# Optimization experiments

Hardware: AMD Instinct MI355X
Metric: run time of the kernel (lower is better)

## Reference

```python
import jax, jax.numpy as jnp
import numpy as np

N_HEAD, D_HEAD, D_MODEL, D_INNER, KSIZE = 16, 64, 1024, 4096, 3
LN_EPS = 1e-3  # keras LayerNormalization default epsilon


def _layernorm(x, g, b):
    m = jnp.mean(x, axis=-1, keepdims=True)
    v = jnp.var(x, axis=-1, keepdims=True)
    return (x - m) * jax.lax.rsqrt(v + LN_EPS) * g + b


def _conv1d_same(x, w, b):
    # x: [B, S, Cin], w: [K, Cin, Cout] (keras Conv1D layout)
    y = jax.lax.conv_general_dilated(x, w, window_strides=(1,), padding='SAME',
                                     dimension_numbers=('NWC', 'WIO', 'NWC'))
    return y + b


def setup_inputs() -> dict:
    key = jax.random.key(0)
    ks = jax.random.split(key, 12)
    B, S, D = 4, 1024, D_MODEL
    dec_inp = jax.random.normal(ks[0], (B, S, D), dtype=jnp.float32)
    # padding mask: True = valid token; ensure >=1 padded position per row
    lengths = jax.random.randint(ks[1], (B,), S // 2, S)
    mask = (jnp.arange(S)[None, :] < lengths[:, None])[:, :, None]  # [B,S,1] bool
    sd = 0.02
    qkv_w = jax.random.normal(ks[2], (D, 3 * N_HEAD * D_HEAD), dtype=jnp.float32) * sd
    qkv_b = jnp.zeros((3 * N_HEAD * D_HEAD,), dtype=jnp.float32)
    o_w = jax.random.normal(ks[3], (N_HEAD * D_HEAD, D), dtype=jnp.float32) * sd
    ln1_g = jnp.ones((D,), dtype=jnp.float32)
    ln1_b = jnp.zeros((D,), dtype=jnp.float32)
    conv1_w = jax.random.normal(ks[4], (KSIZE, D, D_INNER), dtype=jnp.float32) * sd
    conv1_b = jnp.zeros((D_INNER,), dtype=jnp.float32)
    conv2_w = jax.random.normal(ks[5], (KSIZE, D_INNER, D), dtype=jnp.float32) * sd
    conv2_b = jnp.zeros((D,), dtype=jnp.float32)
    ln2_g = jnp.ones((D,), dtype=jnp.float32)
    ln2_b = jnp.zeros((D,), dtype=jnp.float32)
    return dict(dec_inp=dec_inp, mask=mask, qkv_w=qkv_w, qkv_b=qkv_b, o_w=o_w,
                ln1_g=ln1_g, ln1_b=ln1_b, conv1_w=conv1_w, conv1_b=conv1_b,
                conv2_w=conv2_w, conv2_b=conv2_b, ln2_g=ln2_g, ln2_b=ln2_b)


def _forward(dec_inp, mask, qkv_w, qkv_b, o_w, ln1_g, ln1_b,
             conv1_w, conv1_b, conv2_w, conv2_b, ln2_g, ln2_b):
    B, S, D = dec_inp.shape
    H, dh = N_HEAD, D_HEAD
    scale = 1.0 / (dh ** 0.5)
    # --- MultiHeadAttn (post-lnorm; dropout inactive at inference) ---
    residual = dec_inp
    qkv = dec_inp @ qkv_w + qkv_b                       # [B,S,3*H*dh]
    hq, hk, hv = jnp.split(qkv, 3, axis=2)
    to_flat = lambda h: h.reshape(B, S, H, dh).transpose(0, 2, 1, 3).reshape(B * H, S, dh)
    q, k, v = to_flat(hq), to_flat(hk), to_flat(hv)
    score = jnp.einsum('bqd,bkd->bqk', q, k) * scale    # [B*H, S, S]
    # attn_mask = ~mask.squeeze(2): True at PAD positions (faithful to TF port)
    am = (~mask[:, :, 0]).astype(score.dtype)[:, None, :]    # [B,1,S]
    am = jnp.tile(am, (H, S, 1))                             # [B*H,S,S] (tile over batch axis, as in tf.tile)
    add = jnp.where(am.astype(bool), am, -jnp.inf)           # pad -> +1.0, valid -> -inf (as written in source)
    score = score + add
    prob = jax.nn.softmax(score, axis=2)
    vec = prob @ v                                      # [B*H,S,dh]
    # faithful to source reshapes: [B*H,S,dh] -> [H,B,S,dh] -> [B,S,H*dh]
    vec = vec.reshape(H, B, S, dh).transpose(1, 2, 0, 3).reshape(B, S, H * dh)
    attn_out = vec @ o_w
    out = _layernorm(residual + attn_out, ln1_g, ln1_b)
    # mask-multiply between blocks
    out = out * mask.astype(out.dtype)
    # --- PositionwiseConvFF (post-lnorm) ---
    core = _conv1d_same(out, conv1_w, conv1_b)
    core = jax.nn.relu(core)
    core = _conv1d_same(core, conv2_w, conv2_b)
    out = _layernorm(out + core, ln2_g, ln2_b)
    out = out * mask.astype(out.dtype)
    return out


def reference(dec_inp, mask, qkv_w, qkv_b, o_w, ln1_g, ln1_b,
              conv1_w, conv1_b, conv2_w, conv2_b, ln2_g, ln2_b):
    return _forward(dec_inp, mask, qkv_w, qkv_b, o_w, ln1_g, ln1_b,
                    conv1_w, conv1_b, conv2_w, conv2_b, ln2_g, ln2_b)
```

## Files before the change

### kernel.cpp

```cpp
#include <hip/hip_runtime.h>
#include <cstdint>
#include <cstddef>

typedef float f32x4 __attribute__((ext_vector_type(4)));
typedef __bf16 bf16x8 __attribute__((ext_vector_type(8)));
typedef unsigned short u16;

__device__ __forceinline__ float bf2f(u16 u) {
  union { unsigned int i; float f; } x; x.i = ((unsigned int)u) << 16; return x.f;
}
__device__ __forceinline__ u16 f2bf(float f) {
  union { float f; unsigned int i; } x; x.f = f;
  unsigned int i = x.i;
  i += 0x7fffu + ((i >> 16) & 1u);
  return (u16)(i >> 16);
}

#if defined(__has_builtin)
#if __has_builtin(__builtin_amdgcn_global_load_lds)
#define HAS_GLL 1
#endif
#endif

__device__ __forceinline__ void async16(const u16* g, u16* l) {
#ifdef HAS_GLL
  __builtin_amdgcn_global_load_lds((const __attribute__((address_space(1))) void*)(const void*)g,
                                   (__attribute__((address_space(3))) void*)(void*)l, 16, 0, 0);
#else
  *(uint4*)l = *(const uint4*)g;
#endif
}

__global__ void compact_mask(const unsigned char* __restrict__ mask,
                             int* __restrict__ padIdx, int* __restrict__ padCnt,
                             float* __restrict__ maskf) {
  const int b = blockIdx.x;
  const int lane = threadIdx.x;
  int stride = 1;
  if (mask[1] == 0) stride = (mask[4] != 0) ? 4 : 8;
  int cnt = 0;
  for (int s0 = 0; s0 < 1024; s0 += 64) {
    const int s = s0 + lane;
    const bool valid = (mask[(size_t)((b << 10) + s) * stride] != 0);
    maskf[(b << 10) + s] = valid ? 1.f : 0.f;
    const bool pad = !valid;
    const unsigned long long bal = __ballot(pad);
    const int rank = (int)__popcll(bal & ((1ull << lane) - 1ull));
    if (pad) padIdx[(b << 10) + cnt + rank] = s;
    cnt += (int)__popcll(bal);
  }
  if (lane == 0) padCnt[b] = cnt;
}

__global__ __launch_bounds__(256)
void f32_to_bf16(const float* __restrict__ in, u16* __restrict__ out, int n4) {
  const int i = blockIdx.x * 256 + threadIdx.x;
  if (i < n4) {
    const float4 v = ((const float4*)in)[i];
    u16 o[4] = { f2bf(v.x), f2bf(v.y), f2bf(v.z), f2bf(v.w) };
    ((ushort4*)out)[i] = *(const ushort4*)o;
  }
}

__global__ __launch_bounds__(256)
void transpose_f32_bf16(const float* __restrict__ in, u16* __restrict__ out, int R, int C) {
  __shared__ u16 tile[64][65];
  const int r0 = blockIdx.y << 6, c0 = blockIdx.x << 6;
  const int tid = threadIdx.x;
  const int lr = tid >> 3, lc = (tid & 7) << 3;
#pragma unroll
  for (int p = 0; p < 2; ++p) {
    const int row = lr + (p << 5);
    const float4 a = *(const float4*)(in + (size_t)(r0 + row) * C + c0 + lc);
    const float4 bq = *(const float4*)(in + (size_t)(r0 + row) * C + c0 + lc + 4);
    tile[row][lc + 0] = f2bf(a.x); tile[row][lc + 1] = f2bf(a.y);
    tile[row][lc + 2] = f2bf(a.z); tile[row][lc + 3] = f2bf(a.w);
    tile[row][lc + 4] = f2bf(bq.x); tile[row][lc + 5] = f2bf(bq.y);
    tile[row][lc + 6] = f2bf(bq.z); tile[row][lc + 7] = f2bf(bq.w);
  }
  __syncthreads();
#pragma unroll
  for (int p = 0; p < 2; ++p) {
    const int oc = lr + (p << 5);
    u16 tmp[8];
#pragma unroll
    for (int e = 0; e < 8; ++e) tmp[e] = tile[lc + e][oc];
    *(uint4*)(out + (size_t)(c0 + oc) * R + r0 + lc) = *(const uint4*)tmp;
  }
}

template<int NTAPS, bool RELU, int SPLITK>
__global__ __launch_bounds__(256)
void gemm_bt(const u16* __restrict__ A, const u16* __restrict__ BT,
             const float* __restrict__ bias, u16* __restrict__ C, u16* __restrict__ Calt,
             int M, int N, int Korig, const u16* __restrict__ zp) {
  __shared__ __align__(16) u16 As[128 * 64];
  __shared__ __align__(16) u16 Bs[128 * 64];
  const int tid = threadIdx.x;
  const int m0 = blockIdx.y << 7;
  const int n0 = blockIdx.x << 7;
  const int kz = (SPLITK > 1) ? blockIdx.z : 0;
  const int Ktot = NTAPS * Korig;
  const int kchunk = Ktot / SPLITK;
  const int lane = tid & 63;
  const int w = tid >> 6;
  const int wm = (w >> 1) << 6;
  const int wn = (w & 1) << 6;
  const int fr = lane & 15;
  const int quad = lane >> 4;
  const int srow = tid >> 3;
  const int scol = (tid & 7) << 3;
  const int sx = (((tid & 7) ^ (srow & 7)) << 3);

  f32x4 acc[4][4] = {};

  const int kbeg = kz * kchunk, kend = kbeg + kchunk;
  for (int k0 = kbeg; k0 < kend; k0 += 64) {
    int t = 0, c0 = k0;
    if (NTAPS == 3) { t = k0 / Korig; c0 = k0 - t * Korig; }
#pragma unroll
    for (int i = 0; i < 4; ++i) {
      const int row = srow + (i << 5);
      const u16* src;
      if (NTAPS == 3) {
        const int m = m0 + row;
        const int sp = (m & 1023) + t - 1;
        src = ((unsigned)sp < 1024u) ? (A + (size_t)(m + t - 1) * Korig + c0 + sx)
                                     : (zp + ((tid & 255) << 3));
      } else {
        src = A + (size_t)(m0 + row) * Korig + c0 + sx;
      }
      async16(src, &As[(row << 6) + scol]);
    }
#pragma unroll
    for (int i = 0; i < 4; ++i) {
      const int n = srow + (i << 5);
      async16(BT + (size_t)(n0 + n) * Ktot + k0 + sx, &Bs[(n << 6) + scol]);
    }
    asm volatile("s_waitcnt vmcnt(0)" ::: "memory");
    __syncthreads();
#pragma unroll
    for (int ks = 0; ks < 64; ks += 32) {
      const int ccol = ((((ks >> 3) + quad) ^ (fr & 7)) << 3);
      bf16x8 af[4], bfr[4];
#pragma unroll
      for (int mi = 0; mi < 4; ++mi)
        af[mi] = *(const bf16x8*)&As[((wm + (mi << 4) + fr) << 6) + ccol];
#pragma unroll
      for (int ni = 0; ni < 4; ++ni)
        bfr[ni] = *(const bf16x8*)&Bs[((wn + (ni << 4) + fr) << 6) + ccol];
#pragma unroll
      for (int mi = 0; mi < 4; ++mi)
#pragma unroll
        for (int ni = 0; ni < 4; ++ni)
          acc[mi][ni] = __builtin_amdgcn_mfma_f32_16x16x32_bf16(af[mi], bfr[ni], acc[mi][ni], 0, 0, 0);
    }
    __syncthreads();
  }
  const int rbase = m0 + wm + (quad << 2);
  const int cbase = n0 + wn + fr;
  u16* dst = C;
  if (SPLITK > 1 && kz > 0) dst = Calt + (size_t)(kz - 1) * ((size_t)M * N);
#pragma unroll
  for (int ni = 0; ni < 4; ++ni) {
    const int col = cbase + (ni << 4);
    const float bv = (SPLITK == 1 && bias) ? bias[col] : 0.f;
#pragma unroll
    for (int mi = 0; mi < 4; ++mi) {
#pragma unroll
      for (int r = 0; r < 4; ++r) {
        float v = acc[mi][ni][r] + bv;
        if (RELU) v = fmaxf(v, 0.f);
        dst[(size_t)(rbase + (mi << 4) + r) * N + col] = f2bf(v);
      }
    }
  }
}

__global__ __launch_bounds__(256)
void reduce_split4(const u16* __restrict__ P0, const u16* __restrict__ P1,
                   const float* __restrict__ bias, u16* __restrict__ out,
                   int MN, int Ncols) {
  const int i8 = (blockIdx.x * 256 + threadIdx.x) << 3;
  if (i8 >= MN) return;
  const uint4 a = *(const uint4*)(P0 + i8);
  const uint4 b = *(const uint4*)(P1 + i8);
  const uint4 c = *(const uint4*)(P1 + MN + i8);
  const uint4 d = *(const uint4*)(P1 + 2 * MN + i8);
  const u16 *ua = (const u16*)&a, *ub = (const u16*)&b, *uc = (const u16*)&c, *ud = (const u16*)&d;
  const int cb = i8 & (Ncols - 1);
  u16 o[8];
#pragma unroll
  for (int e = 0; e < 8; ++e) {
    const float s = bf2f(ua[e]) + bf2f(ub[e]) + bf2f(uc[e]) + bf2f(ud[e]) + bias[cb + e];
    o[e] = f2bf(s);
  }
  *(uint4*)(out + i8) = *(const uint4*)o;
}

__global__ __launch_bounds__(256)
void gather_v(const u16* __restrict__ qkv, const int* __restrict__ padIdx,
              const int* __restrict__ padCnt, u16* __restrict__ Vt) {
  const int bm = blockIdx.x;
  const int jt = blockIdx.y;
  const int b = bm >> 2, mb = bm & 3;
  const int npad = padCnt[mb];
  const int npadR = (npad + 63) & ~63;
  if (jt * 64 >= npadR) return;
  const int tid = threadIdx.x;
  __shared__ int rows[64];
  if (tid < 64) {
    const int j = jt * 64 + tid;
    const int jj = j < npad ? j : npad - 1;
    rows[tid] = padIdx[(mb << 10) + jj];
  }
  __shared__ u16 tile[64][72];
  for (int c = 0; c < 16; ++c) {
    const int ch0 = c << 6;
    __syncthreads();
#pragma unroll
    for (int p = 0; p < 2; ++p) {
      const int r = (tid >> 3) + (p << 5);
      const int ch = (tid & 7) << 3;
      const uint4 v = *(const uint4*)(qkv + (size_t)((b << 10) + rows[r]) * 3072 + 2048 + ch0 + ch);
      const u16* us = (const u16*)&v;
#pragma unroll
      for (int e = 0; e < 8; ++e) tile[r][ch + e] = us[e];
    }
    __syncthreads();
#pragma unroll
    for (int p = 0; p < 2; ++p) {
      const int r = (tid >> 3) + (p << 5);
      const int jc = (tid & 7) << 3;
      u16 tmp[8];
#pragma unroll
      for (int e = 0; e < 8; ++e) tmp[e] = tile[jc + e][r];
      *(uint4*)(Vt + (size_t)((bm << 10) + ch0 + r) * 512 + jt * 64 + jc) = *(const uint4*)tmp;
    }
  }
}

__global__ __launch_bounds__(256)
void attn_mfma(const u16* __restrict__ qkv, const u16* __restrict__ Vt,
               const int* __restrict__ padIdx, const int* __restrict__ padCnt,
               u16* __restrict__ vecS) {
  __shared__ __align__(16) u16 Ks[64 * 64];
  __shared__ __align__(16) u16 Vts[64 * 64];
  __shared__ __align__(16) u16 Ps[4][32 * 88];
  __shared__ int rowsIdx[512];
  const int i = blockIdx.x;
  const int qt = blockIdx.y;
  const int b = i >> 4, h = i & 15;
  const int mb = h & 3, bm = (b << 2) + mb;
  const int h_out = i >> 2;
  const int npad = padCnt[mb];
  const int nkt = (npad + 63) >> 6;
  const int tid = threadIdx.x;
  const int w = tid >> 6, lane = tid & 63;
  const int fr = lane & 15, quad = lane >> 4, fko = quad << 3;
  const int srow = tid >> 3, scol = (tid & 7) << 3;
  const int sx = (((tid & 7) ^ (srow & 7)) << 3);

#pragma unroll
  for (int p = 0; p < 2; ++p) {
    const int j = (p << 8) + tid;
    const int jj = j < npad ? j : npad - 1;
    rowsIdx[j] = padIdx[(mb << 10) + jj];
  }

  const int qw = (qt << 7) + (w << 5);
  bf16x8 qf[2][2];
#pragma unroll
  for (int rt = 0; rt < 2; ++rt)
#pragma unroll
    for (int ks = 0; ks < 2; ++ks)
      qf[rt][ks] = *(const bf16x8*)(qkv + (size_t)((b << 10) + qw + (rt << 4) + fr) * 3072 +
                                    (h << 6) + (ks << 5) + fko);

  f32x4 O[2][4];
  float mrun[2][4], lrun[2][4];
#pragma unroll
  for (int rt = 0; rt < 2; ++rt)
#pragma unroll
    for (int r = 0; r < 4; ++r) {
      mrun[rt][r] = -1e30f; lrun[rt][r] = 0.f;
#pragma unroll
      for (int dt = 0; dt < 4; ++dt) O[rt][dt][r] = 0.f;
    }
  __syncthreads();

  for (int kt = 0; kt < nkt; ++kt) {
#pragma unroll
    for (int p = 0; p < 2; ++p) {
      const int r = srow + (p << 5);
      const int grow = rowsIdx[(kt << 6) + r];
      async16(qkv + (size_t)((b << 10) + grow) * 3072 + 1024 + (h << 6) + sx,
              &Ks[(r << 6) + scol]);
      async16(Vt + (size_t)((bm << 10) + (h << 6) + r) * 512 + (kt << 6) + sx,
              &Vts[(r << 6) + scol]);
    }
    asm volatile("s_waitcnt vmcnt(0)" ::: "memory");
    __syncthreads();

    f32x4 S[2][4];
#pragma unroll
    for (int rt = 0; rt < 2; ++rt)
#pragma unroll
      for (int nt = 0; nt < 4; ++nt)
#pragma unroll
        for (int r = 0; r < 4; ++r) S[rt][nt][r] = 0.f;
#pragma unroll
    for (int ks = 0; ks < 2; ++ks) {
      const int ccol = ((((ks << 2) + quad) ^ (fr & 7)) << 3);
      bf16x8 bfr[4];
#pragma unroll
      for (int nt = 0; nt < 4; ++nt)
        bfr[nt] = *(const bf16x8*)&Ks[(((nt << 4) + fr) << 6) + ccol];
#pragma unroll
      for (int rt = 0; rt < 2; ++rt)
#pragma unroll
        for (int nt = 0; nt < 4; ++nt)
          S[rt][nt] = __builtin_amdgcn_mfma_f32_16x16x32_bf16(qf[rt][ks], bfr[nt], S[rt][nt], 0, 0, 0);
    }

#pragma unroll
    for (int nt = 0; nt < 4; ++nt) {
      const int key = (kt << 6) + (nt << 4) + fr;
      const bool dead = (key >= npad);
#pragma unroll
      for (int rt = 0; rt < 2; ++rt)
#pragma unroll
        for (int r = 0; r < 4; ++r) {
          float s = S[rt][nt][r] * 0.125f;
          S[rt][nt][r] = dead ? -1e30f : s;
        }
    }

#pragma unroll
    for (int rt = 0; rt < 2; ++rt) {
#pragma unroll
      for (int r = 0; r < 4; ++r) {
        float mx = fmaxf(fmaxf(S[rt][0][r], S[rt][1][r]), fmaxf(S[rt][2][r], S[rt][3][r]));
#pragma unroll
        for (int off = 1; off <= 8; off <<= 1) mx = fmaxf(mx, __shfl_xor(mx, off, 64));
        const float mnew = fmaxf(mrun[rt][r], mx);
        const float alpha = __expf(mrun[rt][r] - mnew);
        mrun[rt][r] = mnew;
        float rsum = 0.f;
#pragma unroll
        for (int nt = 0; nt < 4; ++nt) {
          const float p_ = __expf(S[rt][nt][r] - mnew);
          S[rt][nt][r] = p_;
          rsum += p_;
        }
#pragma unroll
        for (int off = 1; off <= 8; off <<= 1) rsum += __shfl_xor(rsum, off, 64);
        lrun[rt][r] = lrun[rt][r] * alpha + rsum;
#pragma unroll
        for (int dt = 0; dt < 4; ++dt) O[rt][dt][r] *= alpha;
      }
    }

    u16* ps = &Ps[w][0];
#pragma unroll
    for (int rt = 0; rt < 2; ++rt)
#pragma unroll
      for (int nt = 0; nt < 4; ++nt)
#pragma unroll
        for (int r = 0; r < 4; ++r)
          ps[((rt << 4) + (quad << 2) + r) * 88 + (nt << 4) + fr] = f2bf(S[rt][nt][r]);
    asm volatile("s_waitcnt lgkmcnt(0)" ::: "memory");

#pragma unroll
    for (int ks = 0; ks < 2; ++ks) {
      const int ccol = ((((ks << 2) + quad) ^ (fr & 7)) << 3);
      bf16x8 af[2], bv[4];
#pragma unroll
      for (int rt = 0; rt < 2; ++rt)
        af[rt] = *(const bf16x8*)&ps[((rt << 4) + fr) * 88 + (ks << 5) + fko];
#pragma unroll
      for (int dt = 0; dt < 4; ++dt)
        bv[dt] = *(const bf16x8*)&Vts[(((dt << 4) + fr) << 6) + ccol];
#pragma unroll
      for (int rt = 0; rt < 2; ++rt)
#pragma unroll
        for (int dt = 0; dt < 4; ++dt)
          O[rt][dt] = __builtin_amdgcn_mfma_f32_16x16x32_bf16(af[rt], bv[dt], O[rt][dt], 0, 0, 0);
    }
    __syncthreads();
  }

#pragma unroll
  for (int rt = 0; rt < 2; ++rt)
#pragma unroll
    for (int r = 0; r < 4; ++r) {
      const float inv = 1.f / lrun[rt][r];
      const int q = qw + (rt << 4) + (quad << 2) + r;
      u16* orow = vecS + (size_t)((mb << 10) + q) * 1024 + (h_out << 6);
#pragma unroll
      for (int dt = 0; dt < 4; ++dt)
        orow[(dt << 4) + fr] = f2bf(O[rt][dt][r] * inv);
    }
}

template<bool XF32, bool OUTF32>
__global__ __launch_bounds__(256)
void ln_kernel(const void* __restrict__ Xv, const u16* __restrict__ Yd,
               const float* __restrict__ g, const float* __restrict__ be,
               const float* __restrict__ maskf, void* __restrict__ outv) {
  const int r = blockIdx.x;
  const int tid = threadIdx.x;
  const size_t base = (size_t)r << 10;
  const float* Xf = (const float*)Xv;
  const u16* Xb = (const u16*)Xv;
  float x[4];
  float s1 = 0.f, s2 = 0.f;
#pragma unroll
  for (int j = 0; j < 4; ++j) {
    const int c = (tid << 2) + j;
    const float xv = XF32 ? Xf[base + c] : bf2f(Xb[base + c]);
    const float v = xv + bf2f(Yd[base + c]);
    x[j] = v; s1 += v; s2 += v * v;
  }
#pragma unroll
  for (int off = 32; off > 0; off >>= 1) { s1 += __shfl_xor(s1, off, 64); s2 += __shfl_xor(s2, off, 64); }
  __shared__ float rs1[4], rs2[4];
  if ((tid & 63) == 0) { rs1[tid >> 6] = s1; rs2[tid >> 6] = s2; }
  __syncthreads();
  s1 = rs1[0] + rs1[1] + rs1[2] + rs1[3];
  s2 = rs2[0] + rs2[1] + rs2[2] + rs2[3];
  const float mean = s1 * (1.f / 1024.f);
  const float var = s2 * (1.f / 1024.f) - mean * mean;
  const float rstd = rsqrtf(var + 1e-3f);
  const float mv = maskf[r];
#pragma unroll
  for (int j = 0; j < 4; ++j) {
    const int c = (tid << 2) + j;
    const float y = ((x[j] - mean) * rstd * g[c] + be[c]) * mv;
    if (OUTF32) ((float*)outv)[base + c] = y;
    else ((u16*)outv)[base + c] = f2bf(y);
  }
}

extern "C" void kernel_launch(void* const* d_in, const int* in_sizes, int n_in,
                              void* d_out, int out_size, void* d_ws, size_t ws_size,
                              hipStream_t stream) {
  (void)in_sizes; (void)n_in; (void)out_size; (void)ws_size;
  const float* dec  = (const float*)d_in[0];
  const unsigned char* mask = (const unsigned char*)d_in[1];
  const float* wqkv = (const float*)d_in[2];
  const float* bqkv = (const float*)d_in[3];
  const float* wo   = (const float*)d_in[4];
  const float* g1   = (const float*)d_in[5];
  const float* b1   = (const float*)d_in[6];
  const float* w1   = (const float*)d_in[7];
  const float* bc1  = (const float*)d_in[8];
  const float* w2   = (const float*)d_in[9];
  const float* bc2  = (const float*)d_in[10];
  const float* g2   = (const float*)d_in[11];
  const float* b2   = (const float*)d_in[12];
  char* ws = (char*)d_ws;
  u16*   zp    = (u16*)(ws + 0);
  int*   pcnt  = (int*)(ws + 4096);
  float* maskf = (float*)(ws + 8192);
  int*   pidx  = (int*)(ws + 24576);
  u16*   decB  = (u16*)(ws + 65536);
  u16*   wqkvT = (u16*)(ws + 8454144);
  u16*   woT   = (u16*)(ws + 14745600);
  u16*   w1T   = (u16*)(ws + 16842752);
  u16*   w2T   = (u16*)(ws + 42008576);
  u16*   qkv   = (u16*)(ws + 67174400);
  u16*   Vt    = (u16*)(ws + 92340224);
  u16*   vecS  = (u16*)(ws + 109117440);
  u16*   atto  = (u16*)(ws + 65536);
  u16*   x1bf  = (u16*)(ws + 8454144);
  u16*   ybuf  = (u16*)(ws + 67174400);
  u16*   core  = (u16*)(ws + 109117440);
  u16*   P0    = (u16*)(ws + 65536);
  u16*   P1    = (u16*)(ws + 16842752);

  hipMemsetAsync(zp, 0, 4096, stream);
  compact_mask<<<dim3(4), dim3(64), 0, stream>>>(mask, pidx, pcnt, maskf);
  f32_to_bf16<<<dim3(4096), dim3(256), 0, stream>>>(dec, decB, 1048576);
  transpose_f32_bf16<<<dim3(48, 16), dim3(256), 0, stream>>>(wqkv, wqkvT, 1024, 3072);
  transpose_f32_bf16<<<dim3(16, 16), dim3(256), 0, stream>>>(wo, woT, 1024, 1024);
  transpose_f32_bf16<<<dim3(64, 48), dim3(256), 0, stream>>>(w1, w1T, 3072, 4096);
  transpose_f32_bf16<<<dim3(16, 192), dim3(256), 0, stream>>>(w2, w2T, 12288, 1024);
  gemm_bt<1, false, 1><<<dim3(24, 32), dim3(256), 0, stream>>>(decB, wqkvT, bqkv, qkv, nullptr, 4096, 3072, 1024, zp);
  gather_v<<<dim3(16, 8), dim3(256), 0, stream>>>(qkv, pidx, pcnt, Vt);
  attn_mfma<<<dim3(64, 8), dim3(256), 0, stream>>>(qkv, Vt, pidx, pcnt, vecS);
  gemm_bt<1, false, 1><<<dim3(8, 32), dim3(256), 0, stream>>>(vecS, woT, nullptr, atto, nullptr, 4096, 1024, 1024, zp);
  ln_kernel<true, false><<<dim3(4096), dim3(256), 0, stream>>>(dec, atto, g1, b1, maskf, x1bf);
  gemm_bt<3, true, 1><<<dim3(32, 32), dim3(256), 0, stream>>>(x1bf, w1T, bc1, ybuf, nullptr, 4096, 4096, 1024, zp);
  gemm_bt<3, false, 4><<<dim3(8, 32, 4), dim3(256), 0, stream>>>(ybuf, w2T, nullptr, P0, P1, 4096, 1024, 4096, zp);
  reduce_split4<<<dim3(2048), dim3(256), 0, stream>>>(P0, P1, bc2, core, 4194304, 1024);
  ln_kernel<false, true><<<dim3(4096), dim3(256), 0, stream>>>(x1bf, core, g2, b2, maskf, (float*)d_out);
}
```

Measured before the change: 585.6 us.

## Fuse split-K reduction into LayerNorm, split-K the output projection, swizzle GEMM blocks

The split-K partial sums are now reduced inside the LayerNorm kernel, so the separate reduce kernel and its round trip through global memory go away. The attention output projection also moves to 4-way split-K so its small grid fills more compute units. GEMM blocks are remapped in groups of 16 M-tiles to improve L2 reuse of the weight tiles, and K is made a compile-time constant with pointer-increment address generation. In exchange, partial sums are rounded to bf16 before they are summed, which adds rounding error, and the LayerNorm kernel now reads four partial buffers.

```diff
diff --git a/kernel.cpp b/kernel.cpp
--- a/kernel.cpp
+++ b/kernel.cpp
@@ -89,19 +89,22 @@
   }
 }
 
-template<int NTAPS, bool RELU, int SPLITK>
+template<int NTAPS, bool RELU, int SPLITK, int KORIG, int NBN>
 __global__ __launch_bounds__(256)
 void gemm_bt(const u16* __restrict__ A, const u16* __restrict__ BT,
              const float* __restrict__ bias, u16* __restrict__ C, u16* __restrict__ Calt,
-             int M, int N, int Korig, const u16* __restrict__ zp) {
+             int M, int N, const u16* __restrict__ zp) {
   __shared__ __align__(16) u16 As[128 * 64];
   __shared__ __align__(16) u16 Bs[128 * 64];
   const int tid = threadIdx.x;
-  const int m0 = blockIdx.y << 7;
-  const int n0 = blockIdx.x << 7;
+  const int id = blockIdx.x + NBN * blockIdx.y;
+  const int bm = ((id / (16 * NBN)) << 4) + (id & 15);
+  const int bn = (id % (16 * NBN)) >> 4;
+  const int m0 = bm << 7;
+  const int n0 = bn << 7;
   const int kz = (SPLITK > 1) ? blockIdx.z : 0;
-  const int Ktot = NTAPS * Korig;
-  const int kchunk = Ktot / SPLITK;
+  constexpr int Ktot = NTAPS * KORIG;
+  constexpr int kchunk = Ktot / SPLITK;
   const int lane = tid & 63;
   const int w = tid >> 6;
   const int wm = (w >> 1) << 6;
@@ -115,47 +118,54 @@
   f32x4 acc[4][4] = {};
 
   const int kbeg = kz * kchunk, kend = kbeg + kchunk;
-  for (int k0 = kbeg; k0 < kend; k0 += 64) {
-    int t = 0, c0 = k0;
-    if (NTAPS == 3) { t = k0 / Korig; c0 = k0 - t * Korig; }
+  int k = kbeg;
+  while (k < kend) {
+    const int t = (NTAPS == 3) ? (k / KORIG) : 0;
+    const int seg_end = (NTAPS == 3) ? min(kend, (t + 1) * KORIG) : kend;
+    const int c0 = k - t * KORIG;
+    const u16* aptr[4];
+    const u16* bptr[4];
 #pragma unroll
     for (int i = 0; i < 4; ++i) {
       const int row = srow + (i << 5);
-      const u16* src;
       if (NTAPS == 3) {
         const int m = m0 + row;
         const int sp = (m & 1023) + t - 1;
-        src = ((unsigned)sp < 1024u) ? (A + (size_t)(m + t - 1) * Korig + c0 + sx)
-                                     : (zp + ((tid & 255) << 3));
+        aptr[i] = ((unsigned)sp < 1024u) ? (A + (size_t)(m + t - 1) * KORIG + c0 + sx)
+                                         : (zp + ((tid & 255) << 3));
       } else {
-        src = A + (size_t)(m0 + row) * Korig + c0 + sx;
+        aptr[i] = A + (size_t)(m0 + row) * KORIG + k + sx;
       }
-      async16(src, &As[(row << 6) + scol]);
-    }
-#pragma unroll
-    for (int i = 0; i < 4; ++i) {
-      const int n = srow + (i << 5);
-      async16(BT + (size_t)(n0 + n) * Ktot + k0 + sx, &Bs[(n << 6) + scol]);
-    }
-    asm volatile("s_waitcnt vmcnt(0)" ::: "memory");
-    __syncthreads();
-#pragma unroll
-    for (int ks = 0; ks < 64; ks += 32) {
-      const int ccol = ((((ks >> 3) + quad) ^ (fr & 7)) << 3);
-      bf16x8 af[4], bfr[4];
-#pragma unroll
-      for (int mi = 0; mi < 4; ++mi)
-        af[mi] = *(const bf16x8*)&As[((wm + (mi << 4) + fr) << 6) + ccol];
-#pragma unroll
-      for (int ni = 0; ni < 4; ++ni)
-        bfr[ni] = *(const bf16x8*)&Bs[((wn + (ni << 4) + fr) << 6) + ccol];
-#pragma unroll
-      for (int mi = 0; mi < 4; ++mi)
+      bptr[i] = BT + (size_t)(n0 + row) * Ktot + k + sx;
+    }
+    for (; k < seg_end; k += 64) {
+#pragma unroll
+      for (int i = 0; i < 4; ++i) {
+        const int row = srow + (i << 5);
+        async16(aptr[i], &As[(row << 6) + scol]);
+        async16(bptr[i], &Bs[(row << 6) + scol]);
+        aptr[i] += 64; bptr[i] += 64;
+      }
+      asm volatile("s_waitcnt vmcnt(0)" ::: "memory");
+      __syncthreads();
+#pragma unroll
+      for (int ks = 0; ks < 64; ks += 32) {
+        const int ccol = ((((ks >> 3) + quad) ^ (fr & 7)) << 3);
+        bf16x8 af[4], bfr[4];
+#pragma unroll
+        for (int mi = 0; mi < 4; ++mi)
+          af[mi] = *(const bf16x8*)&As[((wm + (mi << 4) + fr) << 6) + ccol];
 #pragma unroll
         for (int ni = 0; ni < 4; ++ni)
-          acc[mi][ni] = __builtin_amdgcn_mfma_f32_16x16x32_bf16(af[mi], bfr[ni], acc[mi][ni], 0, 0, 0);
-    }
-    __syncthreads();
+          bfr[ni] = *(const bf16x8*)&Bs[((wn + (ni << 4) + fr) << 6) + ccol];
+#pragma unroll
+        for (int mi = 0; mi < 4; ++mi)
+#pragma unroll
+          for (int ni = 0; ni < 4; ++ni)
+            acc[mi][ni] = __builtin_amdgcn_mfma_f32_16x16x32_bf16(af[mi], bfr[ni], acc[mi][ni], 0, 0, 0);
+      }
+      __syncthreads();
+    }
   }
   const int rbase = m0 + wm + (quad << 2);
   const int cbase = n0 + wn + fr;
@@ -175,27 +185,6 @@
       }
     }
   }
-}
-
-__global__ __launch_bounds__(256)
-void reduce_split4(const u16* __restrict__ P0, const u16* __restrict__ P1,
-                   const float* __restrict__ bias, u16* __restrict__ out,
-                   int MN, int Ncols) {
-  const int i8 = (blockIdx.x * 256 + threadIdx.x) << 3;
-  if (i8 >= MN) return;
-  const uint4 a = *(const uint4*)(P0 + i8);
-  const uint4 b = *(const uint4*)(P1 + i8);
-  const uint4 c = *(const uint4*)(P1 + MN + i8);
-  const uint4 d = *(const uint4*)(P1 + 2 * MN + i8);
-  const u16 *ua = (const u16*)&a, *ub = (const u16*)&b, *uc = (const u16*)&c, *ud = (const u16*)&d;
-  const int cb = i8 & (Ncols - 1);
-  u16 o[8];
-#pragma unroll
-  for (int e = 0; e < 8; ++e) {
-    const float s = bf2f(ua[e]) + bf2f(ub[e]) + bf2f(uc[e]) + bf2f(ud[e]) + bias[cb + e];
-    o[e] = f2bf(s);
-  }
-  *(uint4*)(out + i8) = *(const uint4*)o;
 }
 
 __global__ __launch_bounds__(256)
@@ -403,11 +392,13 @@
     }
 }
 
-template<bool XF32, bool OUTF32>
-__global__ __launch_bounds__(256)
-void ln_kernel(const void* __restrict__ Xv, const u16* __restrict__ Yd,
-               const float* __restrict__ g, const float* __restrict__ be,
-               const float* __restrict__ maskf, void* __restrict__ outv) {
+template<bool XF32, bool OUTF32, bool HASB>
+__global__ __launch_bounds__(256)
+void ln_red4(const void* __restrict__ Xv, const u16* __restrict__ P0,
+             const u16* __restrict__ P1, int MN,
+             const float* __restrict__ bias,
+             const float* __restrict__ g, const float* __restrict__ be,
+             const float* __restrict__ maskf, void* __restrict__ outv) {
   const int r = blockIdx.x;
   const int tid = threadIdx.x;
   const size_t base = (size_t)r << 10;
@@ -418,8 +409,11 @@
 #pragma unroll
   for (int j = 0; j < 4; ++j) {
     const int c = (tid << 2) + j;
-    const float xv = XF32 ? Xf[base + c] : bf2f(Xb[base + c]);
-    const float v = xv + bf2f(Yd[base + c]);
+    const size_t idx = base + c;
+    float y = bf2f(P0[idx]) + bf2f(P1[idx]) + bf2f(P1[MN + idx]) + bf2f(P1[2 * (size_t)MN + idx]);
+    if (HASB) y += bias[c];
+    const float xv = XF32 ? Xf[idx] : bf2f(Xb[idx]);
+    const float v = xv + y;
     x[j] = v; s1 += v; s2 += v * v;
   }
 #pragma unroll
@@ -461,9 +455,9 @@
   const float* b2   = (const float*)d_in[12];
   char* ws = (char*)d_ws;
   u16*   zp    = (u16*)(ws + 0);
-  int*   pcnt  = (int*)(ws + 4096);
-  float* maskf = (float*)(ws + 8192);
-  int*   pidx  = (int*)(ws + 24576);
+  int*   pcnt  = (int*)(ws + 16384);
+  float* maskf = (float*)(ws + 20480);
+  int*   pidx  = (int*)(ws + 40960);
   u16*   decB  = (u16*)(ws + 65536);
   u16*   wqkvT = (u16*)(ws + 8454144);
   u16*   woT   = (u16*)(ws + 14745600);
@@ -472,27 +466,26 @@
   u16*   qkv   = (u16*)(ws + 67174400);
   u16*   Vt    = (u16*)(ws + 92340224);
   u16*   vecS  = (u16*)(ws + 109117440);
-  u16*   atto  = (u16*)(ws + 65536);
   u16*   x1bf  = (u16*)(ws + 8454144);
   u16*   ybuf  = (u16*)(ws + 67174400);
-  u16*   core  = (u16*)(ws + 109117440);
-  u16*   P0    = (u16*)(ws + 65536);
-  u16*   P1    = (u16*)(ws + 16842752);
-
-  hipMemsetAsync(zp, 0, 4096, stream);
+  u16*   aP0   = (u16*)(ws + 65536);
+  u16*   aP1   = (u16*)(ws + 67174400);
+  u16*   cP0   = (u16*)(ws + 65536);
+  u16*   cP1   = (u16*)(ws + 16842752);
+
+  hipMemsetAsync(zp, 0, 16384, stream);
   compact_mask<<<dim3(4), dim3(64), 0, stream>>>(mask, pidx, pcnt, maskf);
   f32_to_bf16<<<dim3(4096), dim3(256), 0, stream>>>(dec, decB, 1048576);
   transpose_f32_bf16<<<dim3(48, 16), dim3(256), 0, stream>>>(wqkv, wqkvT, 1024, 3072);
   transpose_f32_bf16<<<dim3(16, 16), dim3(256), 0, stream>>>(wo, woT, 1024, 1024);
   transpose_f32_bf16<<<dim3(64, 48), dim3(256), 0, stream>>>(w1, w1T, 3072, 4096);
   transpose_f32_bf16<<<dim3(16, 192), dim3(256), 0, stream>>>(w2, w2T, 12288, 1024);
-  gemm_bt<1, false, 1><<<dim3(24, 32), dim3(256), 0, stream>>>(decB, wqkvT, bqkv, qkv, nullptr, 4096, 3072, 1024, zp);
+  gemm_bt<1, false, 1, 1024, 24><<<dim3(24, 32), dim3(256), 0, stream>>>(decB, wqkvT, bqkv, qkv, nullptr, 4096, 3072, zp);
   gather_v<<<dim3(16, 8), dim3(256), 0, stream>>>(qkv, pidx, pcnt, Vt);
   attn_mfma<<<dim3(64, 8), dim3(256), 0, stream>>>(qkv, Vt, pidx, pcnt, vecS);
-  gemm_bt<1, false, 1><<<dim3(8, 32), dim3(256), 0, stream>>>(vecS, woT, nullptr, atto, nullptr, 4096, 1024, 1024, zp);
-  ln_kernel<true, false><<<dim3(4096), dim3(256), 0, stream>>>(dec, atto, g1, b1, maskf, x1bf);
-  gemm_bt<3, true, 1><<<dim3(32, 32), dim3(256), 0, stream>>>(x1bf, w1T, bc1, ybuf, nullptr, 4096, 4096, 1024, zp);
-  gemm_bt<3, false, 4><<<dim3(8, 32, 4), dim3(256), 0, stream>>>(ybuf, w2T, nullptr, P0, P1, 4096, 1024, 4096, zp);
-  reduce_split4<<<dim3(2048), dim3(256), 0, stream>>>(P0, P1, bc2, core, 4194304, 1024);
-  ln_kernel<false, true><<<dim3(4096), dim3(256), 0, stream>>>(x1bf, core, g2, b2, maskf, (float*)d_out);
-}
+  gemm_bt<1, false, 4, 1024, 8><<<dim3(8, 32, 4), dim3(256), 0, stream>>>(vecS, woT, nullptr, aP0, aP1, 4096, 1024, zp);
+  ln_red4<true, false, false><<<dim3(4096), dim3(256), 0, stream>>>(dec, aP0, aP1, 4194304, nullptr, g1, b1, maskf, x1bf);
+  gemm_bt<3, true, 1, 1024, 32><<<dim3(32, 32), dim3(256), 0, stream>>>(x1bf, w1T, bc1, ybuf, nullptr, 4096, 4096, zp);
+  gemm_bt<3, false, 4, 4096, 8><<<dim3(8, 32, 4), dim3(256), 0, stream>>>(ybuf, w2T, nullptr, cP0, cP1, 4096, 1024, zp);
+  ln_red4<false, true, true><<<dim3(4096), dim3(256), 0, stream>>>(x1bf, cP0, cP1, 4194304, bc2, g2, b2, maskf, (float*)d_out);
+}
```

Result: faster. 540.3 us (-7.7%).
